# Kernel optimization log

Measured on AMD Instinct MI355X. Metric: run time of the kernel, lower is better.

Reference implementation:

```python
import jax, jax.numpy as jnp
import numpy as np
from jax import lax

N_NODES = 116
N_EDGES = 1160
D_FEAT = 653  # SAGEConv in/out channels (last dim)


def _sage_max(x, src, dst, w_l, w_r, b):
    # PyG SAGEConv(aggr='max'): out = lin_l(max_j x_j) + lin_r(x)
    # x: [N, C, F]; aggregation over incoming edges per target node.
    msgs = x[src]  # [E, C, F]
    agg = jax.ops.segment_max(msgs, dst, num_segments=N_NODES)
    agg = jnp.where(jnp.isfinite(agg), agg, 0.0)  # empty segments -> 0 (PyG behavior)
    return jnp.einsum('ncf,gf->ncg', agg, w_l) + b + jnp.einsum('ncf,gf->ncg', x, w_r)


def setup_inputs() -> dict:
    key = jax.random.key(0)
    ks = jax.random.split(key, 16)
    inp = {}
    inp['x'] = jax.random.normal(ks[0], (N_NODES, 64, 657), dtype=jnp.float32)
    inp['edge_index'] = jax.random.randint(ks[1], (2, N_EDGES), 0, N_NODES, dtype=jnp.int64)
    # Conv1d(64 -> 256, kernel=5, groups=4): weight [256, 16, 5]
    inp['conv_w'] = jax.random.normal(ks[2], (256, 16, 5), dtype=jnp.float32) * 0.05
    inp['conv_b'] = jax.random.normal(ks[3], (256,), dtype=jnp.float32) * 0.05
    s = 1.0 / np.sqrt(D_FEAT)
    inp['sage_wl'] = jax.random.normal(ks[4], (D_FEAT, D_FEAT), dtype=jnp.float32) * s
    inp['sage_wr'] = jax.random.normal(ks[5], (D_FEAT, D_FEAT), dtype=jnp.float32) * s
    inp['sage_b'] = jnp.zeros((D_FEAT,), dtype=jnp.float32)
    inp['fc1_w'] = jax.random.normal(ks[6], (128, D_FEAT), dtype=jnp.float32) * s
    inp['fc1_b'] = jnp.zeros((128,), dtype=jnp.float32)
    inp['fc2_w'] = jax.random.normal(ks[7], (32, 128), dtype=jnp.float32) * (1.0 / np.sqrt(128))
    inp['fc2_b'] = jnp.zeros((32,), dtype=jnp.float32)
    inp['fc3_w'] = jax.random.normal(ks[8], (4, 32), dtype=jnp.float32) * (1.0 / np.sqrt(32))
    inp['fc3_b'] = jnp.zeros((4,), dtype=jnp.float32)
    return inp


def reference(x, edge_index, conv_w, conv_b, sage_wl, sage_wr, sage_b,
              fc1_w, fc1_b, fc2_w, fc2_b, fc3_w, fc3_b):
    # grouped Conv1d: [N,64,657] -> [N,256,653]
    h = lax.conv_general_dilated(
        x, conv_w, window_strides=(1,), padding='VALID',
        dimension_numbers=('NCH', 'OIH', 'NCH'), feature_group_count=4)
    h = h + conv_b[None, :, None]
    src, dst = edge_index[0], edge_index[1]
    for _ in range(3):  # same SAGEConv layer applied three times
        h = _sage_max(h, src, dst, sage_wl, sage_wr, sage_b)
    # global_mean_pool over the single graph (batch all zeros) then squeeze
    h = h.mean(axis=0)  # [256, 653]
    h = jax.nn.gelu(h @ fc1_w.T + fc1_b, approximate=False)
    h = jax.nn.gelu(h @ fc2_w.T + fc2_b, approximate=False)
    h = h @ fc3_w.T + fc3_b  # [256, 4]
    return jax.nn.softmax(h, axis=1)
```

## Files before the change

### kernel.cpp

```cpp
#include <hip/hip_runtime.h>
#include <hip/hip_bf16.h>
#include <math.h>

#define NN 116
#define NE 1160
#define CCH 256
#define FF 653
#define KP 672
#define MM (NN*CCH)
#define NPAD 768
#define NT6 (NPAD/128)
#define SZH ((size_t)MM*KP)

typedef unsigned short ushort;
typedef short bf16x8 __attribute__((ext_vector_type(8)));
typedef float f32x4 __attribute__((ext_vector_type(4)));

__device__ __forceinline__ float bfbits_to_f(ushort u) {
    unsigned int w = ((unsigned int)u) << 16;
    return __uint_as_float(w);
}
__device__ __forceinline__ ushort f_to_bfbits(float f) {
    unsigned int u = __float_as_uint(f);
    u += 0x7FFFu + ((u >> 16) & 1u);
    return (ushort)(u >> 16);
}

__device__ __forceinline__ void gl_lds16(const void* g, void* l) {
    __builtin_amdgcn_global_load_lds(
        (const __attribute__((address_space(1))) unsigned int*)g,
        (__attribute__((address_space(3))) unsigned int*)l, 16, 0, 0);
}

__global__ void build_csr_k(const int* __restrict__ ei, int* __restrict__ off,
                            int* __restrict__ lst) {
    __shared__ int s_cnt[NN];
    __shared__ int s_off[NN + 1];
    int t = threadIdx.x;
    for (int i = t; i < NN; i += blockDim.x) s_cnt[i] = 0;
    __syncthreads();
    for (int e = t; e < NE; e += blockDim.x) atomicAdd(&s_cnt[ei[NE + e]], 1);
    __syncthreads();
    if (t == 0) {
        s_off[0] = 0;
        for (int i = 0; i < NN; ++i) s_off[i + 1] = s_off[i] + s_cnt[i];
    }
    __syncthreads();
    for (int i = t; i < NN; i += blockDim.x) { off[i] = s_off[i]; s_cnt[i] = 0; }
    if (t == 0) off[NN] = s_off[NN];
    __syncthreads();
    for (int e = t; e < NE; e += blockDim.x) {
        int d = ei[NE + e];
        int p = atomicAdd(&s_cnt[d], 1);
        lst[s_off[d] + p] = ei[e];
    }
}

__global__ void build_wc_k(const float* __restrict__ wl, const float* __restrict__ wr,
                           ushort* __restrict__ wc) {
    int idx = blockIdx.x * 256 + threadIdx.x;
    const int total = 2 * NPAD * KP;
    if (idx >= total) return;
    int k = idx % KP;
    int rem = idx / KP;
    int n = rem % NPAD;
    int p = rem / NPAD;
    float v = 0.f;
    if (n < FF && k < FF) v = (p ? wr : wl)[(size_t)n * FF + k];
    wc[idx] = f_to_bfbits(v);
}

__global__ __launch_bounds__(256) void conv1d_k(
    const float* __restrict__ x, const float* __restrict__ w,
    const float* __restrict__ b, ushort* __restrict__ h) {
    const int f  = blockIdx.x * 256 + threadIdx.x;
    if (f >= KP) return;
    const int n  = blockIdx.y;
    const int o0 = blockIdx.z * 16;
    const int g  = o0 >> 6;
    if (f >= FF) {
#pragma unroll
        for (int oo = 0; oo < 16; ++oo)
            h[(size_t)(n * CCH + o0 + oo) * KP + f] = 0;
        return;
    }
    const float* xp = x + ((size_t)n * 64 + g * 16) * 657 + f;
    const float* wq = w + o0 * 80;
    float acc[16];
#pragma unroll
    for (int oo = 0; oo < 16; ++oo) acc[oo] = b[o0 + oo];
#pragma unroll
    for (int i = 0; i < 16; ++i) {
        float xv[5];
#pragma unroll
        for (int k = 0; k < 5; ++k) xv[k] = xp[i * 657 + k];
#pragma unroll
        for (int oo = 0; oo < 16; ++oo) {
            const float* wp = wq + oo * 80 + i * 5;
            acc[oo] = fmaf(xv[0], wp[0], acc[oo]);
            acc[oo] = fmaf(xv[1], wp[1], acc[oo]);
            acc[oo] = fmaf(xv[2], wp[2], acc[oo]);
            acc[oo] = fmaf(xv[3], wp[3], acc[oo]);
            acc[oo] = fmaf(xv[4], wp[4], acc[oo]);
        }
    }
#pragma unroll
    for (int oo = 0; oo < 16; ++oo)
        h[(size_t)(n * CCH + o0 + oo) * KP + f] = f_to_bfbits(acc[oo]);
}

__global__ void seg_max_k(const ushort* __restrict__ h, ushort* __restrict__ agg,
                          const int* __restrict__ off, const int* __restrict__ lst) {
    int j = blockIdx.x * 256 + threadIdx.x;
    int c = j / 84;
    int chunk = j % 84;
    int n = blockIdx.y;
    int o0 = off[n], o1 = off[n + 1];
    size_t dsti = ((size_t)(n * CCH + c)) * KP + chunk * 8;
    if (o0 == o1) {
        *(uint4*)(agg + dsti) = make_uint4(0, 0, 0, 0);
        return;
    }
    float m[8];
#pragma unroll
    for (int i = 0; i < 8; ++i) m[i] = -3.4e38f;
    for (int e = o0; e < o1; ++e) {
        int s = lst[e];
        const uint4 v = *(const uint4*)(h + ((size_t)(s * CCH + c)) * KP + chunk * 8);
        unsigned int u[4] = {v.x, v.y, v.z, v.w};
#pragma unroll
        for (int q = 0; q < 4; ++q) {
            float lo = __uint_as_float(u[q] << 16);
            float hi = __uint_as_float(u[q] & 0xFFFF0000u);
            m[2*q]   = fmaxf(m[2*q],   lo);
            m[2*q+1] = fmaxf(m[2*q+1], hi);
        }
    }
    unsigned int o[4];
#pragma unroll
    for (int q = 0; q < 4; ++q) {
        unsigned int a = __float_as_uint(m[2*q])   >> 16;
        unsigned int bq = __float_as_uint(m[2*q+1]) & 0xFFFF0000u;
        o[q] = a | bq;
    }
    *(uint4*)(agg + dsti) = make_uint4(o[0], o[1], o[2], o[3]);
}

__global__ void seg_pool_k(const ushort* __restrict__ h, float* __restrict__ part,
                           const int* __restrict__ off, const int* __restrict__ lst) {
    int j = blockIdx.x * 256 + threadIdx.x;
    int c = j / 84;
    int chunk = j % 84;
    int nq = blockIdx.y;
    float s[8];
#pragma unroll
    for (int i = 0; i < 8; ++i) s[i] = 0.f;
    for (int n = nq * 29; n < nq * 29 + 29; ++n) {
        int o0 = off[n], o1 = off[n + 1];
        if (o0 == o1) continue;
        float m[8];
#pragma unroll
        for (int i = 0; i < 8; ++i) m[i] = -3.4e38f;
        for (int e = o0; e < o1; ++e) {
            int sr = lst[e];
            const uint4 v = *(const uint4*)(h + ((size_t)(sr * CCH + c)) * KP + chunk * 8);
            unsigned int u[4] = {v.x, v.y, v.z, v.w};
#pragma unroll
            for (int q = 0; q < 4; ++q) {
                float lo = __uint_as_float(u[q] << 16);
                float hi = __uint_as_float(u[q] & 0xFFFF0000u);
                m[2*q]   = fmaxf(m[2*q],   lo);
                m[2*q+1] = fmaxf(m[2*q+1], hi);
            }
        }
#pragma unroll
        for (int i = 0; i < 8; ++i) s[i] += m[i];
    }
    float* dst = part + ((size_t)(nq * CCH + c)) * KP + chunk * 8;
#pragma unroll
    for (int i = 0; i < 8; ++i) dst[i] = s[i];
}

__global__ void combine_k(const float* __restrict__ part, ushort* __restrict__ aggP) {
    int j = blockIdx.x * 256 + threadIdx.x;
    int c = j / 84;
    int chunk = j % 84;
    const float inv = 1.0f / NN;
#pragma unroll 1
    for (int i = 0; i < 8; ++i) {
        size_t o = ((size_t)c) * KP + chunk * 8 + i;
        float s = part[o] + part[(size_t)CCH * KP + o]
                + part[(size_t)2 * CCH * KP + o] + part[(size_t)3 * CCH * KP + o];
        aggP[o] = f_to_bfbits(s * inv);
    }
}

__global__ void pool_k(const ushort* __restrict__ h, ushort* __restrict__ poolm) {
    int j = blockIdx.x * 256 + threadIdx.x;
    if (j >= 256 * 84) return;
    int c = j / 84;
    int chunk = j % 84;
    float s[8];
#pragma unroll
    for (int i = 0; i < 8; ++i) s[i] = 0.f;
    for (int n = 0; n < NN; ++n) {
        const uint4 v = *(const uint4*)(h + ((size_t)(n * CCH + c)) * KP + chunk * 8);
        unsigned int u[4] = {v.x, v.y, v.z, v.w};
#pragma unroll
        for (int q = 0; q < 4; ++q) {
            s[2*q]   += __uint_as_float(u[q] << 16);
            s[2*q+1] += __uint_as_float(u[q] & 0xFFFF0000u);
        }
    }
    const float inv = 1.0f / NN;
    ushort* dst = poolm + (size_t)c * KP + chunk * 8;
#pragma unroll
    for (int i = 0; i < 8; ++i) dst[i] = f_to_bfbits(s[i] * inv);
}

__global__ __launch_bounds__(256) void sage_gemm_k(
    const ushort* __restrict__ Agg, const ushort* __restrict__ Hcur,
    const ushort* __restrict__ Wc, const float* __restrict__ bias,
    ushort* __restrict__ Hnxt)
{
    __shared__ ushort As[128 * 32];
    __shared__ ushort Bs[128 * 32];
    const int bid = blockIdx.x;
    const int nwg = gridDim.x;
    const int q   = nwg >> 3, r = nwg & 7;
    const int xcd = bid & 7,  jj = bid >> 3;
    const int wgid = (xcd < r ? xcd * (q + 1) : r * (q + 1) + (xcd - r) * q) + jj;
    const int mt = wgid / NT6;
    const int nt = wgid - mt * NT6;
    const int bm = mt * 128;
    const int bn = nt * 128;
    const int tid  = threadIdx.x;
    const int lane = tid & 63;
    const int wid  = tid >> 6;
    const int wm = (wid >> 1) * 64;
    const int wn = (wid & 1) * 64;

    f32x4 acc[4][4];
#pragma unroll
    for (int i = 0; i < 4; ++i)
#pragma unroll
        for (int j = 0; j < 4; ++j) acc[i][j] = 0.f;

    const int srow   = lane >> 2;
    const int schunk = lane & 3;
    const int schk   = (schunk ^ ((srow >> 1) & 3)) * 8;
    ushort* lA = As + wid * 16 * 32;
    ushort* lB = Bs + wid * 16 * 32;
    const int lr  = lane & 15;
    const int cc  = lane >> 4;
    const int kc  = (cc ^ ((lr >> 1) & 3)) * 8;

    for (int pass = 0; pass < 2; ++pass) {
        const ushort* Ab = pass ? Hcur : Agg;
        const ushort* Wb = Wc + (size_t)pass * NPAD * KP;
        for (int k0 = 0; k0 < KP; k0 += 32) {
            const ushort* ga0 = Ab + (size_t)(bm + wid * 16 + srow) * KP + k0 + schk;
            const ushort* gb0 = Wb + (size_t)(bn + wid * 16 + srow) * KP + k0 + schk;
            gl_lds16(ga0, lA);
            gl_lds16(ga0 + (size_t)64 * KP, lA + 64 * 32);
            gl_lds16(gb0, lB);
            gl_lds16(gb0 + (size_t)64 * KP, lB + 64 * 32);
            __syncthreads();
            bf16x8 af[4], bfr[4];
#pragma unroll
            for (int i = 0; i < 4; ++i)
                af[i] = *(const bf16x8*)&As[(wm + i * 16 + lr) * 32 + kc];
#pragma unroll
            for (int j = 0; j < 4; ++j)
                bfr[j] = *(const bf16x8*)&Bs[(wn + j * 16 + lr) * 32 + kc];
#pragma unroll
            for (int i = 0; i < 4; ++i)
#pragma unroll
                for (int j = 0; j < 4; ++j)
                    acc[i][j] = __builtin_amdgcn_mfma_f32_16x16x32_bf16(
                        af[i], bfr[j], acc[i][j], 0, 0, 0);
            __syncthreads();
        }
    }
    const int lg = lane >> 4;
#pragma unroll
    for (int j = 0; j < 4; ++j) {
        int n = bn + wn + j * 16 + lr;
        if (n >= KP) continue;
        bool valid = n < FF;
        float bv = valid ? bias[n] : 0.f;
#pragma unroll
        for (int i = 0; i < 4; ++i) {
#pragma unroll
            for (int rgi = 0; rgi < 4; ++rgi) {
                int m = bm + wm + i * 16 + lg * 4 + rgi;
                float v = valid ? (acc[i][j][rgi] + bv) : 0.f;
                Hnxt[(size_t)m * KP + n] = f_to_bfbits(v);
            }
        }
    }
}

__device__ __forceinline__ float gelu_exact(float v) {
    return 0.5f * v * (1.0f + erff(v * 0.70710678118654752f));
}

__global__ void head_k(const ushort* __restrict__ pool,
                       const float* __restrict__ w1, const float* __restrict__ b1,
                       const float* __restrict__ w2, const float* __restrict__ b2,
                       const float* __restrict__ w3, const float* __restrict__ b3,
                       float* __restrict__ out) {
    __shared__ float row[FF];
    __shared__ float h1[128];
    __shared__ float h2[32];
    __shared__ float sc[4];
    const int c = blockIdx.x;
    const int t = threadIdx.x;
    for (int i = t; i < FF; i += 128) row[i] = bfbits_to_f(pool[(size_t)c * KP + i]);
    __syncthreads();
    {
        const float* wp = w1 + (size_t)t * FF;
        float s = b1[t];
        for (int i = 0; i < FF; ++i) s = fmaf(row[i], wp[i], s);
        h1[t] = gelu_exact(s);
    }
    __syncthreads();
    if (t < 32) {
        const float* wp = w2 + (size_t)t * 128;
        float s = b2[t];
#pragma unroll
        for (int i = 0; i < 128; ++i) s = fmaf(h1[i], wp[i], s);
        h2[t] = gelu_exact(s);
    }
    __syncthreads();
    if (t < 4) {
        const float* wp = w3 + (size_t)t * 32;
        float s = b3[t];
#pragma unroll
        for (int i = 0; i < 32; ++i) s = fmaf(h2[i], wp[i], s);
        sc[t] = s;
    }
    __syncthreads();
    if (t < 4) {
        float mx = fmaxf(fmaxf(sc[0], sc[1]), fmaxf(sc[2], sc[3]));
        float e0 = __expf(sc[0] - mx), e1 = __expf(sc[1] - mx);
        float e2 = __expf(sc[2] - mx), e3 = __expf(sc[3] - mx);
        float inv = 1.0f / (e0 + e1 + e2 + e3);
        float ev = (t == 0) ? e0 : (t == 1) ? e1 : (t == 2) ? e2 : e3;
        out[(size_t)c * 4 + t] = ev * inv;
    }
}

extern "C" void kernel_launch(void* const* d_in, const int* in_sizes, int n_in,
                              void* d_out, int out_size, void* d_ws, size_t ws_size,
                              hipStream_t stream) {
    const float* x      = (const float*)d_in[0];
    const int*   ei     = (const int*)  d_in[1];
    const float* conv_w = (const float*)d_in[2];
    const float* conv_b = (const float*)d_in[3];
    const float* wl     = (const float*)d_in[4];
    const float* wr     = (const float*)d_in[5];
    const float* sb     = (const float*)d_in[6];
    const float* fc1w   = (const float*)d_in[7];
    const float* fc1b   = (const float*)d_in[8];
    const float* fc2w   = (const float*)d_in[9];
    const float* fc2b   = (const float*)d_in[10];
    const float* fc3w   = (const float*)d_in[11];
    const float* fc3b   = (const float*)d_in[12];
    float* out = (float*)d_out;

    ushort* hA   = (ushort*)d_ws;
    ushort* hB   = hA + SZH;
    ushort* agg  = hB + SZH;
    ushort* wc   = agg + SZH;
    ushort* aggP = wc + (size_t)2 * NPAD * KP;
    ushort* h2P  = aggP + (size_t)CCH * KP;
    ushort* poolt= h2P + (size_t)CCH * KP;
    float*  part = (float*)(poolt + (size_t)CCH * KP);
    int*    off  = (int*)(part + (size_t)4 * CCH * KP);
    int*    lst  = off + 128;

    build_csr_k<<<1, 256, 0, stream>>>(ei, off, lst);
    build_wc_k<<<(2 * NPAD * KP + 255) / 256, 256, 0, stream>>>(wl, wr, wc);
    {
        dim3 cgrid(3, NN, 16);
        conv1d_k<<<cgrid, 256, 0, stream>>>(x, conv_w, conv_b, hA);
    }

    dim3 sg_grid(84, NN);
    seg_max_k<<<sg_grid, 256, 0, stream>>>(hA, agg, off, lst);
    sage_gemm_k<<<MM / 128 * NT6, 256, 0, stream>>>(agg, hA, wc, sb, hB);
    seg_max_k<<<sg_grid, 256, 0, stream>>>(hB, agg, off, lst);
    sage_gemm_k<<<MM / 128 * NT6, 256, 0, stream>>>(agg, hB, wc, sb, hA);
    seg_pool_k<<<dim3(84, 4), 256, 0, stream>>>(hA, part, off, lst);
    combine_k<<<84, 256, 0, stream>>>(part, aggP);
    pool_k<<<84, 256, 0, stream>>>(hA, h2P);
    sage_gemm_k<<<(CCH / 128) * NT6, 256, 0, stream>>>(aggP, h2P, wc, sb, poolt);
    head_k<<<CCH, 128, 0, stream>>>(poolt, fc1w, fc1b, fc2w, fc2b, fc3w, fc3b, out);
}
```

Baseline: 656.0 us.

## Stage per-channel node tiles in LDS for segment max and fuse pooling kernels

Measured after the change: 622.0 us. -5.2%, faster.

```diff
diff --git a/kernel.cpp b/kernel.cpp
--- a/kernel.cpp
+++ b/kernel.cpp
@@ -109,113 +109,111 @@
         h[(size_t)(n * CCH + o0 + oo) * KP + f] = f_to_bfbits(acc[oo]);
 }
 
-__global__ void seg_max_k(const ushort* __restrict__ h, ushort* __restrict__ agg,
-                          const int* __restrict__ off, const int* __restrict__ lst) {
-    int j = blockIdx.x * 256 + threadIdx.x;
-    int c = j / 84;
-    int chunk = j % 84;
-    int n = blockIdx.y;
-    int o0 = off[n], o1 = off[n + 1];
-    size_t dsti = ((size_t)(n * CCH + c)) * KP + chunk * 8;
-    if (o0 == o1) {
-        *(uint4*)(agg + dsti) = make_uint4(0, 0, 0, 0);
-        return;
-    }
-    float m[8];
-#pragma unroll
-    for (int i = 0; i < 8; ++i) m[i] = -3.4e38f;
-    for (int e = o0; e < o1; ++e) {
-        int s = lst[e];
-        const uint4 v = *(const uint4*)(h + ((size_t)(s * CCH + c)) * KP + chunk * 8);
-        unsigned int u[4] = {v.x, v.y, v.z, v.w};
-#pragma unroll
-        for (int q = 0; q < 4; ++q) {
-            float lo = __uint_as_float(u[q] << 16);
-            float hi = __uint_as_float(u[q] & 0xFFFF0000u);
-            m[2*q]   = fmaxf(m[2*q],   lo);
-            m[2*q+1] = fmaxf(m[2*q+1], hi);
-        }
-    }
-    unsigned int o[4];
-#pragma unroll
-    for (int q = 0; q < 4; ++q) {
-        unsigned int a = __float_as_uint(m[2*q])   >> 16;
-        unsigned int bq = __float_as_uint(m[2*q+1]) & 0xFFFF0000u;
-        o[q] = a | bq;
-    }
-    *(uint4*)(agg + dsti) = make_uint4(o[0], o[1], o[2], o[3]);
-}
-
-__global__ void seg_pool_k(const ushort* __restrict__ h, float* __restrict__ part,
-                           const int* __restrict__ off, const int* __restrict__ lst) {
-    int j = blockIdx.x * 256 + threadIdx.x;
-    int c = j / 84;
-    int chunk = j % 84;
-    int nq = blockIdx.y;
-    float s[8];
-#pragma unroll
-    for (int i = 0; i < 8; ++i) s[i] = 0.f;
-    for (int n = nq * 29; n < nq * 29 + 29; ++n) {
+__global__ __launch_bounds__(256) void seg_maxT_k(
+    const ushort* __restrict__ h, ushort* __restrict__ agg,
+    const int* __restrict__ off, const int* __restrict__ lst) {
+    __shared__ uint4 sh[NN * 4];
+    const int c  = blockIdx.x;
+    const int f0 = blockIdx.y * 32;
+    const int t  = threadIdx.x;
+    for (int u = t; u < NN * 4; u += 256) {
+        int n = u >> 2, sub = u & 3;
+        sh[u] = *(const uint4*)(h + ((size_t)(n * CCH + c)) * KP + f0 + sub * 8);
+    }
+    __syncthreads();
+    for (int u = t; u < NN * 4; u += 256) {
+        int n = u >> 2, sub = u & 3;
         int o0 = off[n], o1 = off[n + 1];
-        if (o0 == o1) continue;
+        uint4 outv;
+        if (o0 == o1) {
+            outv = make_uint4(0, 0, 0, 0);
+        } else {
+            float m[8];
+#pragma unroll
+            for (int i = 0; i < 8; ++i) m[i] = -3.4e38f;
+            for (int e = o0; e < o1; ++e) {
+                int s = lst[e];
+                uint4 v = sh[s * 4 + sub];
+                unsigned int uu[4] = {v.x, v.y, v.z, v.w};
+#pragma unroll
+                for (int q = 0; q < 4; ++q) {
+                    float lo = __uint_as_float(uu[q] << 16);
+                    float hi = __uint_as_float(uu[q] & 0xFFFF0000u);
+                    m[2*q]   = fmaxf(m[2*q],   lo);
+                    m[2*q+1] = fmaxf(m[2*q+1], hi);
+                }
+            }
+            unsigned int o[4];
+#pragma unroll
+            for (int q = 0; q < 4; ++q) {
+                unsigned int a  = __float_as_uint(m[2*q])   >> 16;
+                unsigned int bq = __float_as_uint(m[2*q+1]) & 0xFFFF0000u;
+                o[q] = a | bq;
+            }
+            outv = make_uint4(o[0], o[1], o[2], o[3]);
+        }
+        *(uint4*)(agg + ((size_t)(n * CCH + c)) * KP + f0 + sub * 8) = outv;
+    }
+}
+
+__global__ __launch_bounds__(256) void seg_pool2_k(
+    const ushort* __restrict__ h, ushort* __restrict__ aggP,
+    ushort* __restrict__ h2P,
+    const int* __restrict__ off, const int* __restrict__ lst) {
+    __shared__ uint4 sh[NN * 4];
+    __shared__ float pm[NN][32];
+    const int c  = blockIdx.x;
+    const int f0 = blockIdx.y * 32;
+    const int t  = threadIdx.x;
+    for (int u = t; u < NN * 4; u += 256) {
+        int n = u >> 2, sub = u & 3;
+        sh[u] = *(const uint4*)(h + ((size_t)(n * CCH + c)) * KP + f0 + sub * 8);
+    }
+    __syncthreads();
+    for (int u = t; u < NN * 4; u += 256) {
+        int n = u >> 2, sub = u & 3;
+        int o0 = off[n], o1 = off[n + 1];
         float m[8];
-#pragma unroll
-        for (int i = 0; i < 8; ++i) m[i] = -3.4e38f;
-        for (int e = o0; e < o1; ++e) {
-            int sr = lst[e];
-            const uint4 v = *(const uint4*)(h + ((size_t)(sr * CCH + c)) * KP + chunk * 8);
-            unsigned int u[4] = {v.x, v.y, v.z, v.w};
-#pragma unroll
-            for (int q = 0; q < 4; ++q) {
-                float lo = __uint_as_float(u[q] << 16);
-                float hi = __uint_as_float(u[q] & 0xFFFF0000u);
-                m[2*q]   = fmaxf(m[2*q],   lo);
-                m[2*q+1] = fmaxf(m[2*q+1], hi);
+        if (o0 == o1) {
+#pragma unroll
+            for (int i = 0; i < 8; ++i) m[i] = 0.f;
+        } else {
+#pragma unroll
+            for (int i = 0; i < 8; ++i) m[i] = -3.4e38f;
+            for (int e = o0; e < o1; ++e) {
+                int s = lst[e];
+                uint4 v = sh[s * 4 + sub];
+                unsigned int uu[4] = {v.x, v.y, v.z, v.w};
+#pragma unroll
+                for (int q = 0; q < 4; ++q) {
+                    float lo = __uint_as_float(uu[q] << 16);
+                    float hi = __uint_as_float(uu[q] & 0xFFFF0000u);
+                    m[2*q]   = fmaxf(m[2*q],   lo);
+                    m[2*q+1] = fmaxf(m[2*q+1], hi);
+                }
             }
-        }
-#pragma unroll
-        for (int i = 0; i < 8; ++i) s[i] += m[i];
-    }
-    float* dst = part + ((size_t)(nq * CCH + c)) * KP + chunk * 8;
-#pragma unroll
-    for (int i = 0; i < 8; ++i) dst[i] = s[i];
-}
-
-__global__ void combine_k(const float* __restrict__ part, ushort* __restrict__ aggP) {
-    int j = blockIdx.x * 256 + threadIdx.x;
-    int c = j / 84;
-    int chunk = j % 84;
-    const float inv = 1.0f / NN;
-#pragma unroll 1
-    for (int i = 0; i < 8; ++i) {
-        size_t o = ((size_t)c) * KP + chunk * 8 + i;
-        float s = part[o] + part[(size_t)CCH * KP + o]
-                + part[(size_t)2 * CCH * KP + o] + part[(size_t)3 * CCH * KP + o];
-        aggP[o] = f_to_bfbits(s * inv);
-    }
-}
-
-__global__ void pool_k(const ushort* __restrict__ h, ushort* __restrict__ poolm) {
-    int j = blockIdx.x * 256 + threadIdx.x;
-    if (j >= 256 * 84) return;
-    int c = j / 84;
-    int chunk = j % 84;
-    float s[8];
-#pragma unroll
-    for (int i = 0; i < 8; ++i) s[i] = 0.f;
-    for (int n = 0; n < NN; ++n) {
-        const uint4 v = *(const uint4*)(h + ((size_t)(n * CCH + c)) * KP + chunk * 8);
-        unsigned int u[4] = {v.x, v.y, v.z, v.w};
-#pragma unroll
-        for (int q = 0; q < 4; ++q) {
-            s[2*q]   += __uint_as_float(u[q] << 16);
-            s[2*q+1] += __uint_as_float(u[q] & 0xFFFF0000u);
-        }
-    }
-    const float inv = 1.0f / NN;
-    ushort* dst = poolm + (size_t)c * KP + chunk * 8;
-#pragma unroll
-    for (int i = 0; i < 8; ++i) dst[i] = f_to_bfbits(s[i] * inv);
+#pragma unroll
+            for (int i = 0; i < 8; ++i)
+                m[i] = __uint_as_float(__float_as_uint(m[i]) & 0xFFFF0000u);
+        }
+#pragma unroll
+        for (int i = 0; i < 8; ++i) pm[n][sub * 8 + i] = m[i];
+    }
+    __syncthreads();
+    if (t < 32) {
+        const float inv = 1.0f / NN;
+        float sa = 0.f, s2 = 0.f;
+        for (int n = 0; n < NN; ++n) {
+            sa += pm[n][t];
+            uint4 v = sh[n * 4 + (t >> 3)];
+            unsigned int w = ((const unsigned int*)&v)[(t >> 1) & 3];
+            float hv = (t & 1) ? __uint_as_float(w & 0xFFFF0000u)
+                               : __uint_as_float(w << 16);
+            s2 += hv;
+        }
+        aggP[(size_t)c * KP + f0 + t] = f_to_bfbits(sa * inv);
+        h2P [(size_t)c * KP + f0 + t] = f_to_bfbits(s2 * inv);
+    }
 }
 
 __global__ __launch_bounds__(256) void sage_gemm_k(
@@ -376,8 +374,7 @@
     ushort* aggP = wc + (size_t)2 * NPAD * KP;
     ushort* h2P  = aggP + (size_t)CCH * KP;
     ushort* poolt= h2P + (size_t)CCH * KP;
-    float*  part = (float*)(poolt + (size_t)CCH * KP);
-    int*    off  = (int*)(part + (size_t)4 * CCH * KP);
+    int*    off  = (int*)(poolt + (size_t)CCH * KP);
     int*    lst  = off + 128;
 
     build_csr_k<<<1, 256, 0, stream>>>(ei, off, lst);
@@ -387,14 +384,12 @@
         conv1d_k<<<cgrid, 256, 0, stream>>>(x, conv_w, conv_b, hA);
     }
 
-    dim3 sg_grid(84, NN);
-    seg_max_k<<<sg_grid, 256, 0, stream>>>(hA, agg, off, lst);
+    dim3 tg(CCH, KP / 32);
+    seg_maxT_k<<<tg, 256, 0, stream>>>(hA, agg, off, lst);
     sage_gemm_k<<<MM / 128 * NT6, 256, 0, stream>>>(agg, hA, wc, sb, hB);
-    seg_max_k<<<sg_grid, 256, 0, stream>>>(hB, agg, off, lst);
+    seg_maxT_k<<<tg, 256, 0, stream>>>(hB, agg, off, lst);
     sage_gemm_k<<<MM / 128 * NT6, 256, 0, stream>>>(agg, hB, wc, sb, hA);
-    seg_pool_k<<<dim3(84, 4), 256, 0, stream>>>(hA, part, off, lst);
-    combine_k<<<84, 256, 0, stream>>>(part, aggP);
-    pool_k<<<84, 256, 0, stream>>>(hA, h2P);
+    seg_pool2_k<<<tg, 256, 0, stream>>>(hA, aggP, h2P, off, lst);
     sage_gemm_k<<<(CCH / 128) * NT6, 256, 0, stream>>>(aggP, h2P, wc, sb, poolt);
     head_k<<<CCH, 128, 0, stream>>>(poolt, fc1w, fc1b, fc2w, fc2b, fc3w, fc3b, out);
 }
```
